# Kernel tuning notes

Measured on AMD Instinct MI355X. Metric: run time of the kernel, lower is better.

The kernel has to match this reference:

```python
import jax, jax.numpy as jnp
import numpy as np
import math

QDIM = KDIM = VDIM = 1024
EMBED = 64   # per-head dim F
HEAD = 16
OUTDIM = 1024
S, N = 2048, 4


def setup_inputs() -> dict:
    key = jax.random.key(0)
    ks = jax.random.split(key, 12)
    d = HEAD * EMBED
    def lin(kw, kb, fan_in, fan_out):
        bound = 1.0 / math.sqrt(fan_in)
        W = jax.random.uniform(kw, (fan_in, fan_out), jnp.float32, -bound, bound)
        b = jax.random.uniform(kb, (fan_out,), jnp.float32, -bound, bound)
        return W, b
    wq_w, wq_b = lin(ks[0], ks[1], QDIM, d)
    wk_w, wk_b = lin(ks[2], ks[3], KDIM, d)
    wv_w, wv_b = lin(ks[4], ks[5], VDIM, d)
    wo_w, wo_b = lin(ks[6], ks[7], d, OUTDIM)
    query = jax.random.normal(ks[8], (S, N, QDIM), jnp.float32)
    key_t = jax.random.normal(ks[9], (S, N, KDIM), jnp.float32)
    value = jax.random.normal(ks[10], (S, N, VDIM), jnp.float32)
    return {"query": query, "key": key_t, "value": value,
            "wq_w": wq_w, "wq_b": wq_b, "wk_w": wk_w, "wk_b": wk_b,
            "wv_w": wv_w, "wv_b": wv_b, "wo_w": wo_w, "wo_b": wo_b}


def reference(query, key, value, wq_w, wq_b, wk_w, wk_b, wv_w, wv_b, wo_w, wo_b):
    F = EMBED
    head = HEAD
    S1, Nq, _ = query.shape
    Sk, Nk, _ = key.shape
    q = query @ wq_w + wq_b            # (S1, N, head*F)
    k = key   @ wk_w + wk_b            # (S,  N, head*F)
    v = value @ wv_w + wv_b            # (S,  N, head*F)
    # view(S, -1, F).transpose(0,1): merge (N, head) -> batch axis B = N*head
    q = q.reshape(S1, Nq * head, F).transpose(1, 0, 2)  # (B, S1, F)
    k = k.reshape(Sk, Nk * head, F).transpose(1, 0, 2)  # (B, S,  F)
    v = v.reshape(Sk, Nk * head, F).transpose(1, 0, 2)  # (B, S,  F)
    scores = jnp.einsum('bif,bjf->bij', q / jnp.sqrt(jnp.float32(F)), k)  # (B, S1, S)
    attn = jax.nn.softmax(scores, axis=-1)
    out = jnp.einsum('bij,bjf->bif', attn, v)           # (B, S1, F)
    out = out.transpose(1, 0, 2).reshape(S1, Nq, head * F)
    return out @ wo_w + wo_b           # (S1, N, outdim)
```

## Files before the change

### kernel.cpp

```cpp
#include <hip/hip_runtime.h>
#include <hip/hip_bf16.h>

#define S_LEN 2048
#define NBATCH 4
#define DMODEL 1024
#define FDIM 64
#define NHEAD 16
#define BHEADS 64
#define MROWS 8192

typedef __attribute__((ext_vector_type(4))) float f32x4;
typedef __attribute__((ext_vector_type(8))) short s16x8;

static __device__ __forceinline__ unsigned short f2bf(float f) {
  union { float f; unsigned u; } v; v.f = f;
  unsigned r = v.u + 0x7fffu + ((v.u >> 16) & 1u);
  return (unsigned short)(r >> 16);
}

#define GLD16(gaddr, laddr)                                            \
  __builtin_amdgcn_global_load_lds(                                    \
      (__attribute__((address_space(1))) void*)(void*)(gaddr),         \
      (__attribute__((address_space(3))) void*)(laddr), 16, 0, 0)

__global__ __launch_bounds__(256) void transpose_w_kernel(
    const float* __restrict__ W, unsigned short* __restrict__ Wt) {
  __shared__ float tile[32][33];
  const int tx = threadIdx.x & 31, ty = threadIdx.x >> 5;
  const int bk = blockIdx.x * 32, bn = blockIdx.y * 32;
#pragma unroll
  for (int i = 0; i < 32; i += 8)
    tile[ty + i][tx] = W[(size_t)(bk + ty + i) * DMODEL + bn + tx];
  __syncthreads();
#pragma unroll
  for (int i = 0; i < 32; i += 8)
    Wt[(size_t)(bn + ty + i) * DMODEL + bk + tx] = f2bf(tile[tx][ty + i]);
}

__global__ __launch_bounds__(256) void convert_kernel(
    const float* __restrict__ in, unsigned short* __restrict__ out) {
  const size_t i = (size_t)blockIdx.x * 256 + threadIdx.x;
  const float4 a = ((const float4*)in)[2 * i];
  const float4 b = ((const float4*)in)[2 * i + 1];
  s16x8 o;
  o[0] = f2bf(a.x); o[1] = f2bf(a.y); o[2] = f2bf(a.z); o[3] = f2bf(a.w);
  o[4] = f2bf(b.x); o[5] = f2bf(b.y); o[6] = f2bf(b.z); o[7] = f2bf(b.w);
  ((s16x8*)out)[i] = o;
}

template <int MODE>
__global__ __launch_bounds__(256, 2) void gemm_kernel(
    const unsigned short* __restrict__ A, const unsigned short* __restrict__ Bt,
    const float* __restrict__ bias, void* __restrict__ outp, float scale) {
  __shared__ unsigned short As[128 * 64];
  __shared__ unsigned short Bs[128 * 64];
  const int tid = threadIdx.x;
  const int lane = tid & 63;
  const int wv = tid >> 6;
  const int wm = (tid >> 7) & 1;
  const int wn = (tid >> 6) & 1;
  const int lg = lane >> 4;
  const int ll = lane & 15;
  const int m0 = blockIdx.x * 128;
  const int n0 = blockIdx.y * 128;

  f32x4 acc[4][4] = {};

  const size_t lane_off =
      (size_t)(lane >> 3) * (DMODEL * 2) + (size_t)(lane & 7) * 16;
  const char* ag = (const char*)(A + (size_t)(m0 + wv * 32) * DMODEL) + lane_off;
  const char* bg = (const char*)(Bt + (size_t)(n0 + wv * 32) * DMODEL) + lane_off;
  char* al = (char*)As + wv * 32 * 128;
  char* bl = (char*)Bs + wv * 32 * 128;

  for (int kt = 0; kt < DMODEL; kt += 64) {
    const size_t kb = (size_t)kt * 2;
#pragma unroll
    for (int c = 0; c < 4; ++c) {
      GLD16(ag + kb + (size_t)c * 8 * DMODEL * 2, al + c * 8 * 128);
      GLD16(bg + kb + (size_t)c * 8 * DMODEL * 2, bl + c * 8 * 128);
    }
    __syncthreads();
#pragma unroll
    for (int ks = 0; ks < 2; ++ks) {
      const int kk = ks * 32 + (lg << 3);
      s16x8 af[4], bfr[4];
#pragma unroll
      for (int mi = 0; mi < 4; ++mi)
        af[mi] = *(const s16x8*)((const char*)As +
                                 (wm * 64 + mi * 16 + ll) * 128 + kk * 2);
#pragma unroll
      for (int ni = 0; ni < 4; ++ni)
        bfr[ni] = *(const s16x8*)((const char*)Bs +
                                  (wn * 64 + ni * 16 + ll) * 128 + kk * 2);
#pragma unroll
      for (int mi = 0; mi < 4; ++mi)
#pragma unroll
        for (int ni = 0; ni < 4; ++ni)
          acc[mi][ni] = __builtin_amdgcn_mfma_f32_16x16x32_bf16(
              af[mi], bfr[ni], acc[mi][ni], 0, 0, 0);
    }
    __syncthreads();
  }

#pragma unroll
  for (int mi = 0; mi < 4; ++mi) {
#pragma unroll
    for (int ni = 0; ni < 4; ++ni) {
      const int col = n0 + wn * 64 + ni * 16 + ll;
      const int rbase = m0 + wm * 64 + mi * 16 + (lg << 2);
      const float bcol = bias[col];
#pragma unroll
      for (int r = 0; r < 4; ++r) {
        const float v = (acc[mi][ni][r] + bcol) * scale;
        const int rr = rbase + r;
        if (MODE == 2) {
          reinterpret_cast<float*>(outp)[(size_t)rr * DMODEL + col] = v;
        } else {
          const int s = rr >> 2, n = rr & 3, h = col >> 6, f = col & 63;
          const int bh = n * NHEAD + h;
          int idx;
          if (MODE == 0) idx = bh * (S_LEN * FDIM) + s * FDIM + f;
          else           idx = bh * (S_LEN * FDIM) + f * S_LEN + s;
          reinterpret_cast<unsigned short*>(outp)[idx] = f2bf(v);
        }
      }
    }
  }
}

__global__ __launch_bounds__(256, 2) void attn_kernel(
    const unsigned short* __restrict__ Q, const unsigned short* __restrict__ Kt,
    const unsigned short* __restrict__ VT, unsigned short* __restrict__ ctx) {
  __shared__ unsigned short Ks[64 * 64];
  __shared__ unsigned short Vs[64 * 64];
  __shared__ unsigned short Ps[4][16 * 64];
  const int flat = blockIdx.x;
  const int xcd = flat & 7;
  const int idx = flat >> 3;
  const int b = xcd * 8 + (idx >> 5);
  const int qt = idx & 31;
  const int tid = threadIdx.x;
  const int wave = tid >> 6, lane = tid & 63;
  const int lg = lane >> 4, ll = lane & 15;
  const int qrow0 = qt * 64 + wave * 16;

  s16x8 qf[2];
  {
    const unsigned short* qp =
        &Q[((size_t)b * S_LEN + qrow0 + ll) * FDIM + (lg << 3)];
    qf[0] = *reinterpret_cast<const s16x8*>(qp);
    qf[1] = *reinterpret_cast<const s16x8*>(qp + 32);
  }

  const unsigned sx =
      (((unsigned)lane & 7u) << 4) ^ (((unsigned)lane >> 3) << 4);
  const char* kbase = (const char*)Kt + (size_t)b * S_LEN * 128;
  const char* vbase = (const char*)VT + (size_t)b * FDIM * (S_LEN * 2);

  float mrow[4], lrow[4];
  f32x4 o[4] = {};
#pragma unroll
  for (int r = 0; r < 4; ++r) { mrow[r] = -1e30f; lrow[r] = 0.f; }

  for (int kv0 = 0; kv0 < S_LEN; kv0 += 64) {
#pragma unroll
    for (int c = 0; c < 2; ++c) {
      const int rb = (wave * 2 + c) * 8;
      GLD16(kbase + ((size_t)(kv0 + rb + (lane >> 3))) * 128 + sx,
            (char*)Ks + rb * 128);
      GLD16(vbase + ((size_t)(rb + (lane >> 3))) * (S_LEN * 2) +
                (size_t)kv0 * 2 + sx,
            (char*)Vs + rb * 128);
    }
    __syncthreads();

    f32x4 sc[4];
#pragma unroll
    for (int ni = 0; ni < 4; ++ni) {
      const int row = ni * 16 + ll;
      unsigned off0 = (unsigned)((row << 6) + (lg << 3)) * 2u;
      unsigned off1 = off0 + 64u;
      off0 ^= (unsigned)(row & 7) << 4;
      off1 ^= (unsigned)(row & 7) << 4;
      const s16x8 kb0 = *reinterpret_cast<const s16x8*>(
          reinterpret_cast<const char*>(Ks) + off0);
      const s16x8 kb1 = *reinterpret_cast<const s16x8*>(
          reinterpret_cast<const char*>(Ks) + off1);
      f32x4 z = {};
      z = __builtin_amdgcn_mfma_f32_16x16x32_bf16(qf[0], kb0, z, 0, 0, 0);
      sc[ni] = __builtin_amdgcn_mfma_f32_16x16x32_bf16(qf[1], kb1, z, 0, 0, 0);
    }

    float pm[4];
#pragma unroll
    for (int r = 0; r < 4; ++r)
      pm[r] = fmaxf(fmaxf(sc[0][r], sc[1][r]), fmaxf(sc[2][r], sc[3][r]));
#pragma unroll
    for (int r = 0; r < 4; ++r)
#pragma unroll
      for (int d = 1; d < 16; d <<= 1)
        pm[r] = fmaxf(pm[r], __shfl_xor(pm[r], d, 64));
    float fac[4], rs[4];
#pragma unroll
    for (int r = 0; r < 4; ++r) {
      const float mn = fmaxf(mrow[r], pm[r]);
      fac[r] = exp2f(mrow[r] - mn);
      mrow[r] = mn;
      lrow[r] *= fac[r];
      rs[r] = 0.f;
    }
#pragma unroll
    for (int ni = 0; ni < 4; ++ni)
#pragma unroll
      for (int r = 0; r < 4; ++r) o[ni][r] *= fac[r];
#pragma unroll
    for (int ni = 0; ni < 4; ++ni) {
#pragma unroll
      for (int r = 0; r < 4; ++r) {
        const float p = exp2f(sc[ni][r] - mrow[r]);
        rs[r] += p;
        const int row = (lg << 2) + r, col = ni * 16 + ll;
        unsigned off = (unsigned)((row << 6) + col) * 2u;
        off ^= (unsigned)(row & 7) << 4;
        *reinterpret_cast<unsigned short*>(
            reinterpret_cast<char*>(Ps[wave]) + off) = f2bf(p);
      }
    }
#pragma unroll
    for (int r = 0; r < 4; ++r) {
#pragma unroll
      for (int d = 1; d < 16; d <<= 1) rs[r] += __shfl_xor(rs[r], d, 64);
      lrow[r] += rs[r];
    }

#pragma unroll
    for (int kk = 0; kk < 2; ++kk) {
      unsigned poff = (unsigned)((ll << 6) + kk * 32 + (lg << 3)) * 2u;
      poff ^= (unsigned)(ll & 7) << 4;
      const s16x8 pa = *reinterpret_cast<const s16x8*>(
          reinterpret_cast<const char*>(Ps[wave]) + poff);
#pragma unroll
      for (int ni = 0; ni < 4; ++ni) {
        const int row = ni * 16 + ll;
        unsigned off = (unsigned)((row << 6) + kk * 32 + (lg << 3)) * 2u;
        off ^= (unsigned)(row & 7) << 4;
        const s16x8 vb = *reinterpret_cast<const s16x8*>(
            reinterpret_cast<const char*>(Vs) + off);
        o[ni] = __builtin_amdgcn_mfma_f32_16x16x32_bf16(pa, vb, o[ni], 0, 0, 0);
      }
    }
    __syncthreads();
  }

  const int n = b >> 4, h = b & 15;
#pragma unroll
  for (int r = 0; r < 4; ++r) {
    const float inv = 1.f / lrow[r];
    const int s = qrow0 + (lg << 2) + r;
#pragma unroll
    for (int ni = 0; ni < 4; ++ni) {
      const int f = ni * 16 + ll;
      ctx[(size_t)(s * NBATCH + n) * DMODEL + h * FDIM + f] =
          f2bf(o[ni][r] * inv);
    }
  }
}

extern "C" void kernel_launch(void* const* d_in, const int* in_sizes, int n_in,
                              void* d_out, int out_size, void* d_ws,
                              size_t ws_size, hipStream_t stream) {
  const float* query = (const float*)d_in[0];
  const float* key_t = (const float*)d_in[1];
  const float* value = (const float*)d_in[2];
  const float* wq_w = (const float*)d_in[3];
  const float* wq_b = (const float*)d_in[4];
  const float* wk_w = (const float*)d_in[5];
  const float* wk_b = (const float*)d_in[6];
  const float* wv_w = (const float*)d_in[7];
  const float* wv_b = (const float*)d_in[8];
  const float* wo_w = (const float*)d_in[9];
  const float* wo_b = (const float*)d_in[10];

  char* ws = (char*)d_ws;
  unsigned short* wtq = (unsigned short*)(ws + (0ull << 20));
  unsigned short* wtk = (unsigned short*)(ws + (2ull << 20));
  unsigned short* wtv = (unsigned short*)(ws + (4ull << 20));
  unsigned short* wto = (unsigned short*)(ws + (6ull << 20));
  unsigned short* cbuf = (unsigned short*)(ws + (8ull << 20));
  unsigned short* qa = (unsigned short*)(ws + (24ull << 20));
  unsigned short* ka = (unsigned short*)(ws + (40ull << 20));
  unsigned short* va = (unsigned short*)(ws + (56ull << 20));
  unsigned short* ctx = (unsigned short*)(ws + (72ull << 20));

  const dim3 blk(256);
  const dim3 tgrid(32, 32);
  hipLaunchKernelGGL(transpose_w_kernel, tgrid, blk, 0, stream, wq_w, wtq);
  hipLaunchKernelGGL(transpose_w_kernel, tgrid, blk, 0, stream, wk_w, wtk);
  hipLaunchKernelGGL(transpose_w_kernel, tgrid, blk, 0, stream, wv_w, wtv);
  hipLaunchKernelGGL(transpose_w_kernel, tgrid, blk, 0, stream, wo_w, wto);

  const dim3 ggrid(MROWS / 128, DMODEL / 128);
  const dim3 cgrid(4096);

  const float qscale = 0.125f * 1.44269504088896340736f;

  hipLaunchKernelGGL(convert_kernel, cgrid, blk, 0, stream, query, cbuf);
  hipLaunchKernelGGL((gemm_kernel<0>), ggrid, blk, 0, stream, cbuf, wtq, wq_b,
                     (void*)qa, qscale);
  hipLaunchKernelGGL(convert_kernel, cgrid, blk, 0, stream, key_t, cbuf);
  hipLaunchKernelGGL((gemm_kernel<0>), ggrid, blk, 0, stream, cbuf, wtk, wk_b,
                     (void*)ka, 1.0f);
  hipLaunchKernelGGL(convert_kernel, cgrid, blk, 0, stream, value, cbuf);
  hipLaunchKernelGGL((gemm_kernel<1>), ggrid, blk, 0, stream, cbuf, wtv, wv_b,
                     (void*)va, 1.0f);

  const dim3 agrid(S_LEN / 64 * BHEADS);
  hipLaunchKernelGGL(attn_kernel, agrid, blk, 0, stream, qa, ka, va, ctx);

  hipLaunchKernelGGL((gemm_kernel<2>), ggrid, blk, 0, stream, ctx, wto, wo_b,
                     d_out, 1.0f);
}
```

Measured before the change: 519.7 us.

## Transpose attention MFMAs to keep P in registers and drop LDS round-trip

Swaps the MFMA operand order so that S^T and O^T are computed, which gives each lane one query row. The softmax max and sum reductions then need only two cross-lane shuffles per block instead of four-step shuffles for each of four rows. Probabilities are packed to bf16 pairs and redistributed through lane shuffles instead of being written to and reread from a per-wave LDS buffer. The output is written as 8-byte vector stores. This removes LDS traffic and reduction work at the cost of extra shuffles and selects.

```diff
diff --git a/kernel.cpp b/kernel.cpp
--- a/kernel.cpp
+++ b/kernel.cpp
@@ -16,6 +16,10 @@
   union { float f; unsigned u; } v; v.f = f;
   unsigned r = v.u + 0x7fffu + ((v.u >> 16) & 1u);
   return (unsigned short)(r >> 16);
+}
+
+static __device__ __forceinline__ unsigned pk2bf(float a, float b) {
+  return (unsigned)f2bf(a) | ((unsigned)f2bf(b) << 16);
 }
 
 #define GLD16(gaddr, laddr)                                            \
@@ -134,7 +138,6 @@
     const unsigned short* __restrict__ VT, unsigned short* __restrict__ ctx) {
   __shared__ unsigned short Ks[64 * 64];
   __shared__ unsigned short Vs[64 * 64];
-  __shared__ unsigned short Ps[4][16 * 64];
   const int flat = blockIdx.x;
   const int xcd = flat & 7;
   const int idx = flat >> 3;
@@ -158,10 +161,11 @@
   const char* kbase = (const char*)Kt + (size_t)b * S_LEN * 128;
   const char* vbase = (const char*)VT + (size_t)b * FDIM * (S_LEN * 2);
 
-  float mrow[4], lrow[4];
+  float m_run = -1e30f, l_run = 0.f;
   f32x4 o[4] = {};
-#pragma unroll
-  for (int r = 0; r < 4; ++r) { mrow[r] = -1e30f; lrow[r] = 0.f; }
+
+  const int shfl_base = ((lg & 1) << 5) + ll;
+  const bool sel_hi = (lg >> 1) != 0;
 
   for (int kv0 = 0; kv0 < S_LEN; kv0 += 64) {
 #pragma unroll
@@ -188,58 +192,61 @@
       const s16x8 kb1 = *reinterpret_cast<const s16x8*>(
           reinterpret_cast<const char*>(Ks) + off1);
       f32x4 z = {};
-      z = __builtin_amdgcn_mfma_f32_16x16x32_bf16(qf[0], kb0, z, 0, 0, 0);
-      sc[ni] = __builtin_amdgcn_mfma_f32_16x16x32_bf16(qf[1], kb1, z, 0, 0, 0);
-    }
-
-    float pm[4];
-#pragma unroll
-    for (int r = 0; r < 4; ++r)
-      pm[r] = fmaxf(fmaxf(sc[0][r], sc[1][r]), fmaxf(sc[2][r], sc[3][r]));
-#pragma unroll
-    for (int r = 0; r < 4; ++r)
-#pragma unroll
-      for (int d = 1; d < 16; d <<= 1)
-        pm[r] = fmaxf(pm[r], __shfl_xor(pm[r], d, 64));
-    float fac[4], rs[4];
-#pragma unroll
-    for (int r = 0; r < 4; ++r) {
-      const float mn = fmaxf(mrow[r], pm[r]);
-      fac[r] = exp2f(mrow[r] - mn);
-      mrow[r] = mn;
-      lrow[r] *= fac[r];
-      rs[r] = 0.f;
-    }
+      z = __builtin_amdgcn_mfma_f32_16x16x32_bf16(kb0, qf[0], z, 0, 0, 0);
+      sc[ni] = __builtin_amdgcn_mfma_f32_16x16x32_bf16(kb1, qf[1], z, 0, 0, 0);
+    }
+
+    float pm0 = fmaxf(fmaxf(sc[0][0], sc[0][1]), fmaxf(sc[0][2], sc[0][3]));
+    float pm1 = fmaxf(fmaxf(sc[1][0], sc[1][1]), fmaxf(sc[1][2], sc[1][3]));
+    float pm2 = fmaxf(fmaxf(sc[2][0], sc[2][1]), fmaxf(sc[2][2], sc[2][3]));
+    float pm3 = fmaxf(fmaxf(sc[3][0], sc[3][1]), fmaxf(sc[3][2], sc[3][3]));
+    float pm = fmaxf(fmaxf(pm0, pm1), fmaxf(pm2, pm3));
+    pm = fmaxf(pm, __shfl_xor(pm, 16, 64));
+    pm = fmaxf(pm, __shfl_xor(pm, 32, 64));
+    const float mn = fmaxf(m_run, pm);
+    const float fac = exp2f(m_run - mn);
+    m_run = mn;
+
+    float rs = 0.f;
 #pragma unroll
     for (int ni = 0; ni < 4; ++ni)
 #pragma unroll
-      for (int r = 0; r < 4; ++r) o[ni][r] *= fac[r];
+      for (int r = 0; r < 4; ++r) {
+        const float p = exp2f(sc[ni][r] - mn);
+        sc[ni][r] = p;
+        rs += p;
+      }
+    rs += __shfl_xor(rs, 16, 64);
+    rs += __shfl_xor(rs, 32, 64);
+    l_run = l_run * fac + rs;
+#pragma unroll
+    for (int ni = 0; ni < 4; ++ni)
+#pragma unroll
+      for (int r = 0; r < 4; ++r) o[ni][r] *= fac;
+
+    unsigned pk[4][2];
 #pragma unroll
     for (int ni = 0; ni < 4; ++ni) {
-#pragma unroll
-      for (int r = 0; r < 4; ++r) {
-        const float p = exp2f(sc[ni][r] - mrow[r]);
-        rs[r] += p;
-        const int row = (lg << 2) + r, col = ni * 16 + ll;
-        unsigned off = (unsigned)((row << 6) + col) * 2u;
-        off ^= (unsigned)(row & 7) << 4;
-        *reinterpret_cast<unsigned short*>(
-            reinterpret_cast<char*>(Ps[wave]) + off) = f2bf(p);
-      }
-    }
-#pragma unroll
-    for (int r = 0; r < 4; ++r) {
-#pragma unroll
-      for (int d = 1; d < 16; d <<= 1) rs[r] += __shfl_xor(rs[r], d, 64);
-      lrow[r] += rs[r];
+      pk[ni][0] = pk2bf(sc[ni][0], sc[ni][1]);
+      pk[ni][1] = pk2bf(sc[ni][2], sc[ni][3]);
     }
 
 #pragma unroll
     for (int kk = 0; kk < 2; ++kk) {
-      unsigned poff = (unsigned)((ll << 6) + kk * 32 + (lg << 3)) * 2u;
-      poff ^= (unsigned)(ll & 7) << 4;
-      const s16x8 pa = *reinterpret_cast<const s16x8*>(
-          reinterpret_cast<const char*>(Ps[wave]) + poff);
+      const int nb = 2 * kk;
+      const unsigned a0 = __shfl(pk[nb][0], shfl_base, 64);
+      const unsigned a1 = __shfl(pk[nb][1], shfl_base, 64);
+      const unsigned c0 = __shfl(pk[nb + 1][0], shfl_base, 64);
+      const unsigned c1 = __shfl(pk[nb + 1][1], shfl_base, 64);
+      const unsigned b0 = __shfl(pk[nb][0], shfl_base + 16, 64);
+      const unsigned b1 = __shfl(pk[nb][1], shfl_base + 16, 64);
+      const unsigned d0 = __shfl(pk[nb + 1][0], shfl_base + 16, 64);
+      const unsigned d1 = __shfl(pk[nb + 1][1], shfl_base + 16, 64);
+      union { s16x8 v; unsigned u[4]; } pb;
+      pb.u[0] = sel_hi ? c0 : a0;
+      pb.u[1] = sel_hi ? c1 : a1;
+      pb.u[2] = sel_hi ? d0 : b0;
+      pb.u[3] = sel_hi ? d1 : b1;
 #pragma unroll
       for (int ni = 0; ni < 4; ++ni) {
         const int row = ni * 16 + ll;
@@ -247,23 +254,24 @@
         off ^= (unsigned)(row & 7) << 4;
         const s16x8 vb = *reinterpret_cast<const s16x8*>(
             reinterpret_cast<const char*>(Vs) + off);
-        o[ni] = __builtin_amdgcn_mfma_f32_16x16x32_bf16(pa, vb, o[ni], 0, 0, 0);
+        o[ni] = __builtin_amdgcn_mfma_f32_16x16x32_bf16(vb, pb.v, o[ni], 0, 0, 0);
       }
     }
     __syncthreads();
   }
 
   const int n = b >> 4, h = b & 15;
-#pragma unroll
-  for (int r = 0; r < 4; ++r) {
-    const float inv = 1.f / lrow[r];
-    const int s = qrow0 + (lg << 2) + r;
-#pragma unroll
-    for (int ni = 0; ni < 4; ++ni) {
-      const int f = ni * 16 + ll;
-      ctx[(size_t)(s * NBATCH + n) * DMODEL + h * FDIM + f] =
-          f2bf(o[ni][r] * inv);
-    }
+  const float inv = 1.f / l_run;
+  const int s = qrow0 + ll;
+  unsigned short* crow = ctx + (size_t)(s * NBATCH + n) * DMODEL + h * FDIM;
+#pragma unroll
+  for (int ni = 0; ni < 4; ++ni) {
+    ushort4 w;
+    w.x = f2bf(o[ni][0] * inv);
+    w.y = f2bf(o[ni][1] * inv);
+    w.z = f2bf(o[ni][2] * inv);
+    w.w = f2bf(o[ni][3] * inv);
+    *reinterpret_cast<ushort4*>(crow + ni * 16 + lg * 4) = w;
   }
 }
 
```

Result: faster. 454.7 us (-12.5%).
